# Kernel tuning notes

Hardware: AMD Instinct MI355X
Metric: run time of the kernel (lower is better)

## Reference

```python
import jax, jax.numpy as jnp
import numpy as np

M, U, H, C, EMB, HID = 4096, 8, 8, 64, 64, 128
N = M * U            # 32768 nodes
E = 131072           # edges
D = H * C            # 512 = heads * hidden_channels
NUM_LAYERS = 4
IN0 = 6              # 2 coords + mask + speed + cost + arrival
SCALE = np.float32(1.0 / np.sqrt(C))

def _lin(x, W, b):
    return x @ W + b

def _transformer_conv(x, src, dst, Wq, bq, Wk, bk, Wv, bv, Ws, bs):
    # PyG TransformerConv: x_j = x[src], x_i = x[dst]; softmax over edges per dst
    n = x.shape[0]
    q = _lin(x, Wq, bq).reshape(n, H, C)
    k = _lin(x, Wk, bk).reshape(n, H, C)
    v = _lin(x, Wv, bv).reshape(n, H, C)
    alpha = jnp.einsum('ehc,ehc->eh', q[dst], k[src]) * SCALE   # [E,H]
    amax = jax.ops.segment_max(alpha, dst, num_segments=n)       # [N,H]
    ex = jnp.exp(alpha - amax[dst])
    denom = jax.ops.segment_sum(ex, dst, num_segments=n)         # [N,H]
    agg = jax.ops.segment_sum(ex[:, :, None] * v[src], dst, num_segments=n)  # [N,H,C]
    out = agg / (denom[:, :, None] + 1e-16)
    return out.reshape(n, D) + _lin(x, Ws, bs)                   # concat heads + root skip

def _forward(mission_coords, uavs_info, speeds, cost_matrix, arrival_times,
             Wq0, bq0, Wk0, bk0, Wv0, bv0, Ws0, bs0,
             Wq, bq, Wk, bk, Wv, bv, Ws, bs,
             fc_W, fc_b, aW1, ab1, aW2, ab2, cW1, cb1, cW2, cb2,
             edge_index, batch, action_mask):
    mc = jnp.broadcast_to(mission_coords[:, None, :], (M, U, 2))
    mk = jnp.broadcast_to(action_mask[:, None, None].astype(jnp.float32), (M, U, 1))
    sp = jnp.broadcast_to(speeds[None, :, None], (M, U, 1))
    cm = cost_matrix.T[:, :, None]
    at = arrival_times.T[:, :, None]
    x = jnp.concatenate([mc, mk, sp, cm, at], axis=-1).reshape(N, IN0)
    src, dst = edge_index[0], edge_index[1]
    x = jax.nn.relu(_transformer_conv(x, src, dst, Wq0, bq0, Wk0, bk0, Wv0, bv0, Ws0, bs0))
    for l in range(NUM_LAYERS - 1):
        x = jax.nn.relu(_transformer_conv(x, src, dst, Wq[l], bq[l], Wk[l], bk[l], Wv[l], bv[l], Ws[l], bs[l]))
    new_batch = jnp.repeat(batch, U)                             # [N]
    sums = jax.ops.segment_sum(x, new_batch, num_segments=1)
    cnts = jax.ops.segment_sum(jnp.ones((N,), x.dtype), new_batch, num_segments=1)
    pooled = sums / cnts[:, None]                                # [1, D]
    emb = _lin(pooled, fc_W, fc_b)                               # [1, EMB]
    emb_exp = jnp.tile(emb, (U, 1))                              # [U, EMB]
    combined = jnp.concatenate([uavs_info, emb_exp, speeds[:, None]], axis=-1)  # [U, EMB+3]
    action_probs = jax.nn.softmax(_lin(jax.nn.relu(_lin(combined, aW1, ab1)), aW2, ab2), axis=-1)
    state_values = _lin(jax.nn.relu(_lin(combined, cW1, cb1)), cW2, cb2)
    return action_probs, state_values

def setup_inputs() -> dict:
    key = jax.random.key(0)
    ks = jax.random.split(key, 40)
    def nrm(i, shape, s=0.05):
        return jax.random.normal(ks[i], shape, jnp.float32) * s
    z = lambda *s: jnp.zeros(s, jnp.float32)
    L = NUM_LAYERS - 1
    inp = dict(
        mission_coords=jax.random.uniform(ks[0], (M, 2), jnp.float32),
        uavs_info=nrm(1, (U, 2), 1.0),
        speeds=jax.random.uniform(ks[2], (U,), jnp.float32) + 0.5,
        cost_matrix=jax.random.uniform(ks[3], (U, M), jnp.float32),
        arrival_times=jax.random.uniform(ks[4], (U, M), jnp.float32),
        edge_index=jax.random.randint(ks[5], (2, E), 0, N),
        batch=jnp.zeros((M,), jnp.int32),
        action_mask=jax.random.randint(ks[6], (M,), 0, 2),
        Wq0=nrm(7, (IN0, D)), bq0=z(D), Wk0=nrm(8, (IN0, D)), bk0=z(D),
        Wv0=nrm(9, (IN0, D)), bv0=z(D), Ws0=nrm(10, (IN0, D)), bs0=z(D),
        Wq=nrm(11, (L, D, D)), bq=z(L, D), Wk=nrm(12, (L, D, D)), bk=z(L, D),
        Wv=nrm(13, (L, D, D)), bv=z(L, D), Ws=nrm(14, (L, D, D)), bs=z(L, D),
        fc_W=nrm(15, (D, EMB)), fc_b=z(EMB),
        aW1=nrm(16, (EMB + 3, HID)), ab1=z(HID), aW2=nrm(17, (HID, M)), ab2=z(M),
        cW1=nrm(18, (EMB + 3, HID)), cb1=z(HID), cW2=nrm(19, (HID, 1)), cb2=z(1),
    )
    return inp

def reference(mission_coords, edge_index, batch, uavs_info, action_mask, speeds,
              cost_matrix, arrival_times,
              Wq0, bq0, Wk0, bk0, Wv0, bv0, Ws0, bs0,
              Wq, bq, Wk, bk, Wv, bv, Ws, bs,
              fc_W, fc_b, aW1, ab1, aW2, ab2, cW1, cb1, cW2, cb2):
    return _forward(mission_coords, uavs_info, speeds, cost_matrix, arrival_times,
                    Wq0, bq0, Wk0, bk0, Wv0, bv0, Ws0, bs0,
                    Wq, bq, Wk, bk, Wv, bv, Ws, bs,
                    fc_W, fc_b, aW1, ab1, aW2, ab2, cW1, cb1, cW2, cb2,
                    edge_index, batch, action_mask)
```

## Files before the change

kernel.cpp:

```cpp
#include <hip/hip_runtime.h>
#include <stdint.h>

typedef unsigned short u16;
typedef __attribute__((ext_vector_type(8))) unsigned short u16x8;
typedef __attribute__((ext_vector_type(8))) __bf16 bf16x8;
typedef __attribute__((ext_vector_type(4))) float f32x4;

#define NNODES 32768
#define NEDGES 131072
#define DDIM 512
#define QK4 2048
#define MM 4096
#define UU 8

__device__ __forceinline__ u16 f2bf(float f) {
    unsigned u = __builtin_bit_cast(unsigned, f);
    u += 0x7FFFu + ((u >> 16) & 1u);
    return (u16)(u >> 16);
}
__device__ __forceinline__ float bf2f(u16 h) {
    return __builtin_bit_cast(float, (unsigned)h << 16);
}

__device__ __forceinline__ void load_lds16(const void* g, void* l) {
    __builtin_amdgcn_global_load_lds((__attribute__((address_space(1))) unsigned int*)(void*)g,
                                     (__attribute__((address_space(3))) unsigned int*)l, 16, 0, 0);
}

__global__ void k_zero(unsigned int* p, int n) {
    int i = blockIdx.x * 256 + threadIdx.x;
    if (i < n) p[i] = 0u;
}

__global__ void k_build_x0(const float* __restrict__ mc, const int* __restrict__ mask,
                           const float* __restrict__ sp, const float* __restrict__ cm,
                           const float* __restrict__ at, float* __restrict__ x0) {
    int node = blockIdx.x * 256 + threadIdx.x;
    if (node >= NNODES) return;
    int m = node >> 3, u = node & 7;
    float* o = x0 + (size_t)node * 6;
    o[0] = mc[m * 2];
    o[1] = mc[m * 2 + 1];
    o[2] = (float)mask[m];
    o[3] = sp[u];
    o[4] = cm[u * MM + m];
    o[5] = at[u * MM + m];
}

__global__ void k_w0cat(const float* __restrict__ Wq0, const float* __restrict__ Wk0,
                        const float* __restrict__ Wv0, const float* __restrict__ Ws0,
                        float* __restrict__ W0cat) {
    int i = blockIdx.x * 256 + threadIdx.x;
    if (i >= 6 * QK4) return;
    int k = i / QK4, n = i % QK4;
    int t = n >> 9, nn = n & 511;
    const float* p = (t == 0) ? Wq0 : (t == 1) ? Wk0 : (t == 2) ? Wv0 : Ws0;
    W0cat[i] = p[k * DDIM + nn];
}

__global__ void k_bcat(const float* __restrict__ bq0, const float* __restrict__ bk0,
                       const float* __restrict__ bv0, const float* __restrict__ bs0,
                       const float* __restrict__ bq, const float* __restrict__ bk,
                       const float* __restrict__ bv, const float* __restrict__ bs,
                       float* __restrict__ b0cat, float* __restrict__ bcat) {
    int i = blockIdx.x * 256 + threadIdx.x;
    if (i >= 4 * QK4) return;
    int n = i & (QK4 - 1);
    int l = i >> 11;
    int t = n >> 9, nn = n & 511;
    if (l == 0) {
        const float* p = (t == 0) ? bq0 : (t == 1) ? bk0 : (t == 2) ? bv0 : bs0;
        b0cat[n] = p[nn];
    } else {
        const float* p = (t == 0) ? bq : (t == 1) ? bk : (t == 2) ? bv : bs;
        bcat[(size_t)(l - 1) * QK4 + n] = p[(l - 1) * DDIM + nn];
    }
}

__global__ void k_wt(const float* __restrict__ Wq, const float* __restrict__ Wk,
                     const float* __restrict__ Wv, const float* __restrict__ Ws,
                     u16* __restrict__ Wt) {
    __shared__ float tile[32][33];
    int q = blockIdx.z;
    int l = q >> 2, t = q & 3;
    const float* src = ((t == 0) ? Wq : (t == 1) ? Wk : (t == 2) ? Wv : Ws) + (size_t)l * DDIM * DDIM;
    int k0 = blockIdx.x * 32, n0 = blockIdx.y * 32;
    int tx = threadIdx.x, ty = threadIdx.y;
#pragma unroll
    for (int r = 0; r < 4; r++) tile[ty + 8 * r][tx] = src[(size_t)(k0 + ty + 8 * r) * DDIM + n0 + tx];
    __syncthreads();
    u16* dst = Wt + (size_t)l * QK4 * DDIM + (size_t)t * DDIM * DDIM;
#pragma unroll
    for (int r = 0; r < 4; r++) {
        int n = n0 + ty + 8 * r;
        dst[(size_t)n * DDIM + k0 + tx] = f2bf(tile[tx][ty + 8 * r]);
    }
}

__global__ void k_count(const int* __restrict__ dst, int* __restrict__ deg) {
    int e = blockIdx.x * 256 + threadIdx.x;
    if (e < NEDGES) atomicAdd(&deg[dst[e]], 1);
}

__global__ __launch_bounds__(1024) void k_scan(const int* __restrict__ deg, int* __restrict__ offs,
                                               int* __restrict__ cursor) {
    __shared__ int sums[1024];
    int t = threadIdx.x;
    int base = t * 32;
    int local[32];
    int s = 0;
#pragma unroll
    for (int i = 0; i < 32; i++) { local[i] = s; s += deg[base + i]; }
    sums[t] = s;
    __syncthreads();
    for (int d = 1; d < 1024; d <<= 1) {
        int v = (t >= d) ? sums[t - d] : 0;
        __syncthreads();
        sums[t] += v;
        __syncthreads();
    }
    int excl = (t == 0) ? 0 : sums[t - 1];
#pragma unroll
    for (int i = 0; i < 32; i++) {
        int o = excl + local[i];
        offs[base + i] = o;
        cursor[base + i] = o;
    }
    if (t == 1023) offs[NNODES] = sums[1023];
}

__global__ void k_scatter(const int* __restrict__ src, const int* __restrict__ dst,
                          int* __restrict__ cursor, int* __restrict__ ssrc) {
    int e = blockIdx.x * 256 + threadIdx.x;
    if (e < NEDGES) {
        int pos = atomicAdd(&cursor[dst[e]], 1);
        ssrc[pos] = src[e];
    }
}

__global__ __launch_bounds__(256) void k_gemm0(const float* __restrict__ x0, const float* __restrict__ W0cat,
                                               const float* __restrict__ b0cat, u16* __restrict__ QKVS) {
    int node = blockIdx.x;
    int t = threadIdx.x;
    float xv[6];
#pragma unroll
    for (int k = 0; k < 6; k++) xv[k] = x0[(size_t)node * 6 + k];
    int n0 = t * 8;
    u16x8 o;
#pragma unroll
    for (int j = 0; j < 8; j++) {
        int n = n0 + j;
        float s = b0cat[n];
#pragma unroll
        for (int k = 0; k < 6; k++) s += xv[k] * W0cat[k * QK4 + n];
        o[j] = f2bf(s);
    }
    *(u16x8*)(QKVS + (size_t)node * QK4 + n0) = o;
}

__global__ __launch_bounds__(256, 4) void k_gemm(const u16* __restrict__ X, const u16* __restrict__ Wt,
                                                 const float* __restrict__ bcat, u16* __restrict__ C) {
    __shared__ __align__(16) u16 smem[2 * 128 * 64];
    u16* As = smem;
    u16* Bs = smem + 128 * 64;
    const int tid = threadIdx.x;
    const int lane = tid & 63;
    const int w = tid >> 6;
    const int wm = w & 1, wn = w >> 1;
    const int bid = blockIdx.x;
    const int xcd = bid & 7;
    const int s = bid >> 3;
    const size_t arow0 = (size_t)(xcd * 32 + (s >> 4)) * 128;
    const size_t brow0 = (size_t)(s & 15) * 128;

    f32x4 acc[4][4];
#pragma unroll
    for (int i = 0; i < 4; i++)
#pragma unroll
        for (int j = 0; j < 4; j++) acc[i][j] = (f32x4){0.f, 0.f, 0.f, 0.f};

    const int la = lane & 7;
    const int quad = lane >> 4;
    const int lm = lane & 15;

    for (int kt = 0; kt < 8; ++kt) {
        const int k0 = kt * 64;
#pragma unroll
        for (int t = 0; t < 4; ++t) {
            int idx = (w * 4 + t) * 64 + lane;
            int m = idx >> 3;
            int c = la ^ (m & 7);
            const u16* ga = X + (arow0 + m) * DDIM + (k0 + c * 8);
            const u16* gb = Wt + (brow0 + m) * DDIM + (k0 + c * 8);
            load_lds16(ga, &As[(size_t)((w * 4 + t) * 64) * 8]);
            load_lds16(gb, &Bs[(size_t)((w * 4 + t) * 64) * 8]);
        }
        __syncthreads();
#pragma unroll
        for (int kk = 0; kk < 2; ++kk) {
            bf16x8 af[4], bfg[4];
            int c = kk * 4 + quad;
#pragma unroll
            for (int i = 0; i < 4; ++i) {
                int m = wm * 64 + i * 16 + lm;
                int slot = m * 8 + (c ^ (m & 7));
                af[i] = *(const bf16x8*)&As[(size_t)slot * 8];
            }
#pragma unroll
            for (int j = 0; j < 4; ++j) {
                int n = wn * 64 + j * 16 + lm;
                int slot = n * 8 + (c ^ (n & 7));
                bfg[j] = *(const bf16x8*)&Bs[(size_t)slot * 8];
            }
#pragma unroll
            for (int i = 0; i < 4; ++i)
#pragma unroll
                for (int j = 0; j < 4; ++j)
                    acc[i][j] = __builtin_amdgcn_mfma_f32_16x16x32_bf16(af[i], bfg[j], acc[i][j], 0, 0, 0);
        }
        __syncthreads();
    }

    float biasv[4];
#pragma unroll
    for (int j = 0; j < 4; ++j) biasv[j] = bcat[brow0 + wn * 64 + j * 16 + lm];

    u16* stg = smem;
    const int chunk = lane & 7;
    const int rrow = lane >> 3;
#pragma unroll
    for (int p = 0; p < 2; ++p) {
        __syncthreads();
#pragma unroll
        for (int ii = 0; ii < 2; ++ii) {
            int i = p * 2 + ii;
#pragma unroll
            for (int j = 0; j < 4; ++j) {
#pragma unroll
                for (int r = 0; r < 4; ++r) {
                    int lr = ii * 16 + quad * 4 + r;
                    int lc = j * 16 + lm;
                    stg[(size_t)(w * 32 + lr) * 72 + lc] = f2bf(acc[i][j][r] + biasv[j]);
                }
            }
        }
        __syncthreads();
#pragma unroll
        for (int it = 0; it < 4; ++it) {
            int row = it * 8 + rrow;
            u16x8 v = *(const u16x8*)&stg[(size_t)(w * 32 + row) * 72 + chunk * 8];
            *(u16x8*)&C[(arow0 + wm * 64 + p * 32 + row) * QK4 + brow0 + wn * 64 + chunk * 8] = v;
        }
    }
}

__global__ __launch_bounds__(256) void k_attn(const u16* __restrict__ QKVS, const int* __restrict__ offs,
                                              const int* __restrict__ ssrc, u16* __restrict__ Xout) {
    const int lane = threadIdx.x & 63;
    const int node = blockIdx.x * 4 + (threadIdx.x >> 6);
    const int c0 = lane * 8;
    const u16x8 qv = *(const u16x8*)(QKVS + (size_t)node * QK4 + c0);
    float qf[8];
#pragma unroll
    for (int j = 0; j < 8; j++) qf[j] = bf2f(qv[j]);
    float m = -INFINITY, l = 0.f;
    float acc[8];
#pragma unroll
    for (int j = 0; j < 8; j++) acc[j] = 0.f;
    const int e0 = offs[node], e1 = offs[node + 1];
    for (int e = e0; e < e1; ++e) {
        int s = ssrc[e];
        const u16x8 kv = *(const u16x8*)(QKVS + (size_t)s * QK4 + 512 + c0);
        const u16x8 vv = *(const u16x8*)(QKVS + (size_t)s * QK4 + 1024 + c0);
        float d = 0.f;
#pragma unroll
        for (int j = 0; j < 8; j++) d += qf[j] * bf2f(kv[j]);
        d += __shfl_xor(d, 1, 64);
        d += __shfl_xor(d, 2, 64);
        d += __shfl_xor(d, 4, 64);
        float a = d * 0.125f;
        float nm = fmaxf(m, a);
        float corr = __expf(m - nm);
        float p = __expf(a - nm);
        l = l * corr + p;
#pragma unroll
        for (int j = 0; j < 8; j++) acc[j] = acc[j] * corr + p * bf2f(vv[j]);
        m = nm;
    }
    float inv = 1.0f / (l + 1e-16f);
    const u16x8 sv = *(const u16x8*)(QKVS + (size_t)node * QK4 + 1536 + c0);
    u16x8 o;
#pragma unroll
    for (int j = 0; j < 8; j++) {
        float r = acc[j] * inv + bf2f(sv[j]);
        o[j] = f2bf(fmaxf(r, 0.f));
    }
    *(u16x8*)(Xout + (size_t)node * DDIM + c0) = o;
}

__global__ __launch_bounds__(256) void k_pool(const u16* __restrict__ X, float* __restrict__ pooled) {
    int t = threadIdx.x;
    int nd0 = blockIdx.x * 512;
    float s0 = 0.f, s1 = 0.f;
    for (int nd = nd0; nd < nd0 + 512; ++nd) {
        s0 += bf2f(X[(size_t)nd * DDIM + t]);
        s1 += bf2f(X[(size_t)nd * DDIM + 256 + t]);
    }
    atomicAdd(&pooled[t], s0);
    atomicAdd(&pooled[t + 256], s1);
}

__global__ __launch_bounds__(1024) void k_heads(const float* __restrict__ pooled, const float* __restrict__ fcW,
                                                const float* __restrict__ fcb, const float* __restrict__ ui,
                                                const float* __restrict__ sp, const float* __restrict__ aW1,
                                                const float* __restrict__ ab1, const float* __restrict__ cW1,
                                                const float* __restrict__ cb1, const float* __restrict__ cW2,
                                                const float* __restrict__ cb2, float* __restrict__ hidden_a,
                                                float* __restrict__ out) {
    __shared__ float spool[512];
    __shared__ float semb[64];
    __shared__ float shc[8][128];
    int t = threadIdx.x;
    if (t < 512) spool[t] = pooled[t] * (1.0f / 32768.0f);
    __syncthreads();
    if (t < 64) {
        float s = fcb[t];
        for (int k = 0; k < 512; k++) s += spool[k] * fcW[k * 64 + t];
        semb[t] = s;
    }
    __syncthreads();
    int u = t >> 7, j = t & 127;
    float u0 = ui[u * 2], u1 = ui[u * 2 + 1], uspd = sp[u];
    float ha = ab1[j] + u0 * aW1[j] + u1 * aW1[128 + j] + uspd * aW1[66 * 128 + j];
    float hc = cb1[j] + u0 * cW1[j] + u1 * cW1[128 + j] + uspd * cW1[66 * 128 + j];
    for (int k = 0; k < 64; k++) {
        float e = semb[k];
        ha += e * aW1[(2 + k) * 128 + j];
        hc += e * cW1[(2 + k) * 128 + j];
    }
    ha = fmaxf(ha, 0.f);
    hc = fmaxf(hc, 0.f);
    hidden_a[u * 128 + j] = ha;
    shc[u][j] = hc;
    __syncthreads();
    if (t < 8) {
        float s = cb2[0];
        for (int k = 0; k < 128; k++) s += shc[t][k] * cW2[k];
        out[NNODES + t] = s;
    }
}

__global__ __launch_bounds__(1024) void k_actor(const float* __restrict__ hidden_a, const float* __restrict__ aW2,
                                                const float* __restrict__ ab2, float* __restrict__ out) {
    __shared__ float h[128];
    __shared__ float red[1024];
    int u = blockIdx.x, t = threadIdx.x;
    if (t < 128) h[t] = hidden_a[u * 128 + t];
    __syncthreads();
    float lg[4];
#pragma unroll
    for (int p = 0; p < 4; p++) {
        int mcol = t + p * 1024;
        float s = ab2[mcol];
        for (int k = 0; k < 128; k++) s += h[k] * aW2[(size_t)k * MM + mcol];
        lg[p] = s;
    }
    float mx = fmaxf(fmaxf(lg[0], lg[1]), fmaxf(lg[2], lg[3]));
    red[t] = mx;
    __syncthreads();
    for (int s2 = 512; s2 > 0; s2 >>= 1) {
        if (t < s2) red[t] = fmaxf(red[t], red[t + s2]);
        __syncthreads();
    }
    mx = red[0];
    __syncthreads();
    float e[4], sum = 0.f;
#pragma unroll
    for (int p = 0; p < 4; p++) {
        e[p] = __expf(lg[p] - mx);
        sum += e[p];
    }
    red[t] = sum;
    __syncthreads();
    for (int s2 = 512; s2 > 0; s2 >>= 1) {
        if (t < s2) red[t] += red[t + s2];
        __syncthreads();
    }
    float inv = 1.0f / red[0];
#pragma unroll
    for (int p = 0; p < 4; p++) out[(size_t)u * MM + t + p * 1024] = e[p] * inv;
}

extern "C" void kernel_launch(void* const* d_in, const int* in_sizes, int n_in,
                              void* d_out, int out_size, void* d_ws, size_t ws_size,
                              hipStream_t stream) {
    const float* mc   = (const float*)d_in[0];
    const float* ui   = (const float*)d_in[1];
    const float* sp   = (const float*)d_in[2];
    const float* cm   = (const float*)d_in[3];
    const float* at   = (const float*)d_in[4];
    const int*   eidx = (const int*)d_in[5];
    const int*   mask = (const int*)d_in[7];
    const float* Wq0 = (const float*)d_in[8];
    const float* bq0 = (const float*)d_in[9];
    const float* Wk0 = (const float*)d_in[10];
    const float* bk0 = (const float*)d_in[11];
    const float* Wv0 = (const float*)d_in[12];
    const float* bv0 = (const float*)d_in[13];
    const float* Ws0 = (const float*)d_in[14];
    const float* bs0 = (const float*)d_in[15];
    const float* Wq = (const float*)d_in[16];
    const float* bq = (const float*)d_in[17];
    const float* Wk = (const float*)d_in[18];
    const float* bk = (const float*)d_in[19];
    const float* Wv = (const float*)d_in[20];
    const float* bv = (const float*)d_in[21];
    const float* Ws = (const float*)d_in[22];
    const float* bs = (const float*)d_in[23];
    const float* fcW = (const float*)d_in[24];
    const float* fcb = (const float*)d_in[25];
    const float* aW1 = (const float*)d_in[26];
    const float* ab1 = (const float*)d_in[27];
    const float* aW2 = (const float*)d_in[28];
    const float* ab2 = (const float*)d_in[29];
    const float* cW1 = (const float*)d_in[30];
    const float* cb1 = (const float*)d_in[31];
    const float* cW2 = (const float*)d_in[32];
    const float* cb2 = (const float*)d_in[33];
    float* out = (float*)d_out;

    const int* esrc = eidx;
    const int* edst = eidx + NEDGES;

    char* ws = (char*)d_ws;
    size_t off = 0;
    auto alloc = [&](size_t bytes) -> void* {
        void* p = ws + off;
        off += (bytes + 255) & ~(size_t)255;
        return p;
    };
    u16*   QKVS  = (u16*)alloc((size_t)NNODES * QK4 * 2);
    u16*   X     = (u16*)alloc((size_t)NNODES * DDIM * 2);
    u16*   Wt    = (u16*)alloc((size_t)3 * QK4 * DDIM * 2);
    float* W0cat = (float*)alloc((size_t)6 * QK4 * 4);
    float* b0cat = (float*)alloc((size_t)QK4 * 4);
    float* bcat  = (float*)alloc((size_t)3 * QK4 * 4);
    float* x0    = (float*)alloc((size_t)NNODES * 6 * 4);
    int*   deg   = (int*)alloc((size_t)NNODES * 4);
    int*   offs  = (int*)alloc((size_t)(NNODES + 1) * 4);
    int*   cursor= (int*)alloc((size_t)NNODES * 4);
    int*   ssrc  = (int*)alloc((size_t)NEDGES * 4);
    float* pooled= (float*)alloc((size_t)512 * 4);
    float* hidden_a = (float*)alloc((size_t)UU * 128 * 4);
    (void)ws_size; (void)in_sizes; (void)n_in; (void)out_size;

    k_zero<<<(NNODES + 255) / 256, 256, 0, stream>>>((unsigned int*)deg, NNODES);
    k_zero<<<2, 256, 0, stream>>>((unsigned int*)pooled, 512);
    k_build_x0<<<NNODES / 256, 256, 0, stream>>>(mc, mask, sp, cm, at, x0);
    k_w0cat<<<(6 * QK4 + 255) / 256, 256, 0, stream>>>(Wq0, Wk0, Wv0, Ws0, W0cat);
    k_bcat<<<(4 * QK4 + 255) / 256, 256, 0, stream>>>(bq0, bk0, bv0, bs0, bq, bk, bv, bs, b0cat, bcat);
    {
        dim3 g(16, 16, 12), b(32, 8);
        k_wt<<<g, b, 0, stream>>>(Wq, Wk, Wv, Ws, Wt);
    }
    k_count<<<NEDGES / 256, 256, 0, stream>>>(edst, deg);
    k_scan<<<1, 1024, 0, stream>>>(deg, offs, cursor);
    k_scatter<<<NEDGES / 256, 256, 0, stream>>>(esrc, edst, cursor, ssrc);

    k_gemm0<<<NNODES, 256, 0, stream>>>(x0, W0cat, b0cat, QKVS);
    k_attn<<<NNODES / 4, 256, 0, stream>>>(QKVS, offs, ssrc, X);

    for (int l = 0; l < 3; ++l) {
        k_gemm<<<4096, 256, 0, stream>>>(X, Wt + (size_t)l * QK4 * DDIM, bcat + (size_t)l * QK4, QKVS);
        k_attn<<<NNODES / 4, 256, 0, stream>>>(QKVS, offs, ssrc, X);
    }

    k_pool<<<64, 256, 0, stream>>>(X, pooled);
    k_heads<<<1, 1024, 0, stream>>>(pooled, fcW, fcb, ui, sp, aW1, ab1, cW1, cb1, cW2, cb2, hidden_a, out);
    k_actor<<<UU, 1024, 0, stream>>>(hidden_a, aW2, ab2, out);
}
```

Baseline: 713.0 us.

## Store K/V in interleaved FP8 to halve attention gather traffic

Splits the fused QKVS buffer into a bf16 Q/skip buffer and an FP8 K/V buffer, where each lane's 8 K values and 8 V values sit together in one 16-byte chunk. The attention kernel then fetches K and V for an edge with a single 16-byte load and converts them with packed FP8 intrinsics. This targets the random per-edge gather bandwidth and the number of load instructions. It lowers K/V precision to FP8, which may affect accuracy. The pool kernel is also vectorised to use 8-wide loads with an LDS reduction over more blocks.

```diff
diff --git a/kernel.cpp b/kernel.cpp
--- a/kernel.cpp
+++ b/kernel.cpp
@@ -5,6 +5,7 @@
 typedef __attribute__((ext_vector_type(8))) unsigned short u16x8;
 typedef __attribute__((ext_vector_type(8))) __bf16 bf16x8;
 typedef __attribute__((ext_vector_type(4))) float f32x4;
+typedef __attribute__((ext_vector_type(2))) float f32x2;
 
 #define NNODES 32768
 #define NEDGES 131072
@@ -20,6 +21,15 @@
 }
 __device__ __forceinline__ float bf2f(u16 h) {
     return __builtin_bit_cast(float, (unsigned)h << 16);
+}
+
+__device__ __forceinline__ void enc8(const float* f, int* lo, int* hi) {
+    int a = __builtin_amdgcn_cvt_pk_fp8_f32(f[0], f[1], 0, false);
+    a = __builtin_amdgcn_cvt_pk_fp8_f32(f[2], f[3], a, true);
+    int b = __builtin_amdgcn_cvt_pk_fp8_f32(f[4], f[5], 0, false);
+    b = __builtin_amdgcn_cvt_pk_fp8_f32(f[6], f[7], b, true);
+    *lo = a;
+    *hi = b;
 }
 
 __device__ __forceinline__ void load_lds16(const void* g, void* l) {
@@ -139,27 +149,45 @@
 }
 
 __global__ __launch_bounds__(256) void k_gemm0(const float* __restrict__ x0, const float* __restrict__ W0cat,
-                                               const float* __restrict__ b0cat, u16* __restrict__ QKVS) {
+                                               const float* __restrict__ b0cat, u16* __restrict__ QS,
+                                               unsigned char* __restrict__ KV8) {
     int node = blockIdx.x;
     int t = threadIdx.x;
     float xv[6];
 #pragma unroll
     for (int k = 0; k < 6; k++) xv[k] = x0[(size_t)node * 6 + k];
     int n0 = t * 8;
-    u16x8 o;
+    float f[8];
 #pragma unroll
     for (int j = 0; j < 8; j++) {
         int n = n0 + j;
         float s = b0cat[n];
 #pragma unroll
         for (int k = 0; k < 6; k++) s += xv[k] * W0cat[k * QK4 + n];
-        o[j] = f2bf(s);
-    }
-    *(u16x8*)(QKVS + (size_t)node * QK4 + n0) = o;
+        f[j] = s;
+    }
+    if (n0 < 512) {
+        u16x8 o;
+#pragma unroll
+        for (int j = 0; j < 8; j++) o[j] = f2bf(f[j]);
+        *(u16x8*)(QS + (size_t)node * 1024 + n0) = o;
+    } else if (n0 < 1536) {
+        int lo, hi;
+        enc8(f, &lo, &hi);
+        int kvcol = (n0 < 1024) ? (n0 - 512) : (n0 - 1024);
+        int ofs = (n0 < 1024) ? 0 : 8;
+        *(int2*)(KV8 + (size_t)node * 1024 + (size_t)(kvcol >> 3) * 16 + ofs) = make_int2(lo, hi);
+    } else {
+        u16x8 o;
+#pragma unroll
+        for (int j = 0; j < 8; j++) o[j] = f2bf(f[j]);
+        *(u16x8*)(QS + (size_t)node * 1024 + 512 + (n0 - 1536)) = o;
+    }
 }
 
 __global__ __launch_bounds__(256, 4) void k_gemm(const u16* __restrict__ X, const u16* __restrict__ Wt,
-                                                 const float* __restrict__ bcat, u16* __restrict__ C) {
+                                                 const float* __restrict__ bcat, u16* __restrict__ QS,
+                                                 unsigned char* __restrict__ KV8) {
     __shared__ __align__(16) u16 smem[2 * 128 * 64];
     u16* As = smem;
     u16* Bs = smem + 128 * 64;
@@ -172,6 +200,7 @@
     const int s = bid >> 3;
     const size_t arow0 = (size_t)(xcd * 32 + (s >> 4)) * 128;
     const size_t brow0 = (size_t)(s & 15) * 128;
+    const int bt = (int)(brow0 >> 7);
 
     f32x4 acc[4][4];
 #pragma unroll
@@ -228,6 +257,7 @@
     u16* stg = smem;
     const int chunk = lane & 7;
     const int rrow = lane >> 3;
+    const int colbase = (int)brow0 + wn * 64 + chunk * 8;
 #pragma unroll
     for (int p = 0; p < 2; ++p) {
         __syncthreads();
@@ -249,17 +279,32 @@
         for (int it = 0; it < 4; ++it) {
             int row = it * 8 + rrow;
             u16x8 v = *(const u16x8*)&stg[(size_t)(w * 32 + row) * 72 + chunk * 8];
-            *(u16x8*)&C[(arow0 + wm * 64 + p * 32 + row) * QK4 + brow0 + wn * 64 + chunk * 8] = v;
+            size_t grow = arow0 + wm * 64 + p * 32 + row;
+            if (bt < 4) {
+                *(u16x8*)&QS[grow * 1024 + colbase] = v;
+            } else if (bt < 12) {
+                float f[8];
+#pragma unroll
+                for (int j = 0; j < 8; j++) f[j] = bf2f(v[j]);
+                int lo, hi;
+                enc8(f, &lo, &hi);
+                int kvcol = (bt < 8) ? (colbase - 512) : (colbase - 1024);
+                int ofs = (bt < 8) ? 0 : 8;
+                *(int2*)(KV8 + grow * 1024 + (size_t)(kvcol >> 3) * 16 + ofs) = make_int2(lo, hi);
+            } else {
+                *(u16x8*)&QS[grow * 1024 + 512 + (colbase - 1536)] = v;
+            }
         }
     }
 }
 
-__global__ __launch_bounds__(256) void k_attn(const u16* __restrict__ QKVS, const int* __restrict__ offs,
-                                              const int* __restrict__ ssrc, u16* __restrict__ Xout) {
+__global__ __launch_bounds__(256) void k_attn(const u16* __restrict__ QS, const unsigned char* __restrict__ KV8,
+                                              const int* __restrict__ offs, const int* __restrict__ ssrc,
+                                              u16* __restrict__ Xout) {
     const int lane = threadIdx.x & 63;
     const int node = blockIdx.x * 4 + (threadIdx.x >> 6);
     const int c0 = lane * 8;
-    const u16x8 qv = *(const u16x8*)(QKVS + (size_t)node * QK4 + c0);
+    const u16x8 qv = *(const u16x8*)(QS + (size_t)node * 1024 + c0);
     float qf[8];
 #pragma unroll
     for (int j = 0; j < 8; j++) qf[j] = bf2f(qv[j]);
@@ -270,11 +315,13 @@
     const int e0 = offs[node], e1 = offs[node + 1];
     for (int e = e0; e < e1; ++e) {
         int s = ssrc[e];
-        const u16x8 kv = *(const u16x8*)(QKVS + (size_t)s * QK4 + 512 + c0);
-        const u16x8 vv = *(const u16x8*)(QKVS + (size_t)s * QK4 + 1024 + c0);
-        float d = 0.f;
-#pragma unroll
-        for (int j = 0; j < 8; j++) d += qf[j] * bf2f(kv[j]);
+        int4 kv = *(const int4*)(KV8 + (size_t)s * 1024 + (size_t)lane * 16);
+        f32x2 k01 = __builtin_amdgcn_cvt_pk_f32_fp8(kv.x, false);
+        f32x2 k23 = __builtin_amdgcn_cvt_pk_f32_fp8(kv.x, true);
+        f32x2 k45 = __builtin_amdgcn_cvt_pk_f32_fp8(kv.y, false);
+        f32x2 k67 = __builtin_amdgcn_cvt_pk_f32_fp8(kv.y, true);
+        float d = qf[0] * k01[0] + qf[1] * k01[1] + qf[2] * k23[0] + qf[3] * k23[1] +
+                  qf[4] * k45[0] + qf[5] * k45[1] + qf[6] * k67[0] + qf[7] * k67[1];
         d += __shfl_xor(d, 1, 64);
         d += __shfl_xor(d, 2, 64);
         d += __shfl_xor(d, 4, 64);
@@ -283,12 +330,22 @@
         float corr = __expf(m - nm);
         float p = __expf(a - nm);
         l = l * corr + p;
-#pragma unroll
-        for (int j = 0; j < 8; j++) acc[j] = acc[j] * corr + p * bf2f(vv[j]);
+        f32x2 v01 = __builtin_amdgcn_cvt_pk_f32_fp8(kv.z, false);
+        f32x2 v23 = __builtin_amdgcn_cvt_pk_f32_fp8(kv.z, true);
+        f32x2 v45 = __builtin_amdgcn_cvt_pk_f32_fp8(kv.w, false);
+        f32x2 v67 = __builtin_amdgcn_cvt_pk_f32_fp8(kv.w, true);
+        acc[0] = acc[0] * corr + p * v01[0];
+        acc[1] = acc[1] * corr + p * v01[1];
+        acc[2] = acc[2] * corr + p * v23[0];
+        acc[3] = acc[3] * corr + p * v23[1];
+        acc[4] = acc[4] * corr + p * v45[0];
+        acc[5] = acc[5] * corr + p * v45[1];
+        acc[6] = acc[6] * corr + p * v67[0];
+        acc[7] = acc[7] * corr + p * v67[1];
         m = nm;
     }
     float inv = 1.0f / (l + 1e-16f);
-    const u16x8 sv = *(const u16x8*)(QKVS + (size_t)node * QK4 + 1536 + c0);
+    const u16x8 sv = *(const u16x8*)(QS + (size_t)node * 1024 + 512 + c0);
     u16x8 o;
 #pragma unroll
     for (int j = 0; j < 8; j++) {
@@ -299,15 +356,29 @@
 }
 
 __global__ __launch_bounds__(256) void k_pool(const u16* __restrict__ X, float* __restrict__ pooled) {
+    __shared__ float red[4][64][8];
     int t = threadIdx.x;
-    int nd0 = blockIdx.x * 512;
-    float s0 = 0.f, s1 = 0.f;
-    for (int nd = nd0; nd < nd0 + 512; ++nd) {
-        s0 += bf2f(X[(size_t)nd * DDIM + t]);
-        s1 += bf2f(X[(size_t)nd * DDIM + 256 + t]);
-    }
-    atomicAdd(&pooled[t], s0);
-    atomicAdd(&pooled[t + 256], s1);
+    int chunk = t & 63;
+    int rofs = t >> 6;
+    float s[8];
+#pragma unroll
+    for (int j = 0; j < 8; j++) s[j] = 0.f;
+    int nd0 = blockIdx.x * 256;
+    for (int nd = nd0 + rofs; nd < nd0 + 256; nd += 4) {
+        u16x8 v = *(const u16x8*)&X[(size_t)nd * DDIM + chunk * 8];
+#pragma unroll
+        for (int j = 0; j < 8; j++) s[j] += bf2f(v[j]);
+    }
+#pragma unroll
+    for (int j = 0; j < 8; j++) red[rofs][chunk][j] = s[j];
+    __syncthreads();
+    if (t < 64) {
+#pragma unroll
+        for (int j = 0; j < 8; j++) {
+            float o = red[0][t][j] + red[1][t][j] + red[2][t][j] + red[3][t][j];
+            atomicAdd(&pooled[t * 8 + j], o);
+        }
+    }
 }
 
 __global__ __launch_bounds__(1024) void k_heads(const float* __restrict__ pooled, const float* __restrict__ fcW,
@@ -439,7 +510,8 @@
         off += (bytes + 255) & ~(size_t)255;
         return p;
     };
-    u16*   QKVS  = (u16*)alloc((size_t)NNODES * QK4 * 2);
+    u16*   QS    = (u16*)alloc((size_t)NNODES * 1024 * 2);
+    unsigned char* KV8 = (unsigned char*)alloc((size_t)NNODES * 1024);
     u16*   X     = (u16*)alloc((size_t)NNODES * DDIM * 2);
     u16*   Wt    = (u16*)alloc((size_t)3 * QK4 * DDIM * 2);
     float* W0cat = (float*)alloc((size_t)6 * QK4 * 4);
@@ -467,15 +539,15 @@
     k_scan<<<1, 1024, 0, stream>>>(deg, offs, cursor);
     k_scatter<<<NEDGES / 256, 256, 0, stream>>>(esrc, edst, cursor, ssrc);
 
-    k_gemm0<<<NNODES, 256, 0, stream>>>(x0, W0cat, b0cat, QKVS);
-    k_attn<<<NNODES / 4, 256, 0, stream>>>(QKVS, offs, ssrc, X);
+    k_gemm0<<<NNODES, 256, 0, stream>>>(x0, W0cat, b0cat, QS, KV8);
+    k_attn<<<NNODES / 4, 256, 0, stream>>>(QS, KV8, offs, ssrc, X);
 
     for (int l = 0; l < 3; ++l) {
-        k_gemm<<<4096, 256, 0, stream>>>(X, Wt + (size_t)l * QK4 * DDIM, bcat + (size_t)l * QK4, QKVS);
-        k_attn<<<NNODES / 4, 256, 0, stream>>>(QKVS, offs, ssrc, X);
-    }
-
-    k_pool<<<64, 256, 0, stream>>>(X, pooled);
+        k_gemm<<<4096, 256, 0, stream>>>(X, Wt + (size_t)l * QK4 * DDIM, bcat + (size_t)l * QK4, QS, KV8);
+        k_attn<<<NNODES / 4, 256, 0, stream>>>(QS, KV8, offs, ssrc, X);
+    }
+
+    k_pool<<<128, 256, 0, stream>>>(X, pooled);
     k_heads<<<1, 1024, 0, stream>>>(pooled, fcW, fcb, ui, sp, aW1, ab1, cW1, cb1, cW2, cb2, hidden_a, out);
     k_actor<<<UU, 1024, 0, stream>>>(hidden_a, aW2, ab2, out);
 }
```

After: 660.7 us. 1.08x faster.
